# Performance work log

Hardware: AMD Instinct MI355X
Metric: run time of the kernel (lower is better)

The kernel has to match this reference:

```python
import jax, jax.numpy as jnp
import numpy as np

NEG_CAUSAL = -1e10  # matches torch buffer triu(ones*-1e10, diag=1)
NEG_PAD = -10000.0
NUM_HEADS = 16


def setup_inputs() -> dict:
    key = jax.random.key(0)
    ks = jax.random.split(key, 6)
    B, S, D = 2, 2048, 1024
    scale = 0.02
    return {
        "hidden_states": jax.random.normal(ks[0], (B, S, D), jnp.float32),
        "attention_mask": jnp.ones((B, S), jnp.float32),
        "Wq": jax.random.normal(ks[1], (D, D), jnp.float32) * scale,
        "bq": jnp.zeros((D,), jnp.float32),
        "Wk": jax.random.normal(ks[2], (D, D), jnp.float32) * scale,
        "bk": jnp.zeros((D,), jnp.float32),
        "Wv": jax.random.normal(ks[3], (D, D), jnp.float32) * scale,
        "bv": jnp.zeros((D,), jnp.float32),
        "Wo": jax.random.normal(ks[4], (D, D), jnp.float32) * scale,
        "bo": jnp.zeros((D,), jnp.float32),
    }


def reference(hidden_states, attention_mask, Wq, bq, Wk, bk, Wv, bv, Wo, bo):
    B, S, D = hidden_states.shape
    H = NUM_HEADS
    hd = D // H

    def heads(x):  # [B,S,D] -> [B,H,S,hd]
        return x.reshape(B, S, H, hd).transpose(0, 2, 1, 3)

    q = heads(hidden_states @ Wq + bq)
    k = heads(hidden_states @ Wk + bk)
    v = heads(hidden_states @ Wv + bv)

    scores = jnp.einsum("bhqd,bhkd->bhqk", q, k) / jnp.sqrt(jnp.float32(hd))
    causal = jnp.triu(jnp.full((S, S), NEG_CAUSAL, jnp.float32), k=1)
    scores = scores + causal
    # additive padding mask: (1 - m) * -10000, broadcast over heads and query pos
    scores = scores + (1.0 - attention_mask)[:, None, None, :] * NEG_PAD

    probs = jax.nn.softmax(scores, axis=-1)
    # dropout p=0.1 is inactive in eval mode (training=False)
    ctx = jnp.einsum("bhqk,bhkd->bhqd", probs, v)
    ctx = ctx.transpose(0, 2, 1, 3).reshape(B, S, D)
    return ctx @ Wo + bo
```

## Files before the change

kernel.cpp:

```cpp
#include <hip/hip_runtime.h>

typedef __attribute__((ext_vector_type(8))) short short8_t;
typedef __attribute__((ext_vector_type(4))) float float4_t;
typedef unsigned short u16;
typedef unsigned int u32;
typedef unsigned long long u64;

__device__ inline u16 f2bf(float x) {
  union { float f; u32 u; } v; v.f = x;
  u32 r = v.u + 0x7FFFu + ((v.u >> 16) & 1u);
  return (u16)(r >> 16);
}
#if __has_builtin(__builtin_amdgcn_cvt_pk_bf16_f32)
typedef __attribute__((ext_vector_type(2))) __bf16 bf162_t;
__device__ inline u32 pk2(float a, float b) {
  union { bf162_t v; u32 u; } cv;
  cv.v = __builtin_amdgcn_cvt_pk_bf16_f32(a, b);
  return cv.u;
}
#else
__device__ inline u32 pk2(float a, float b) {
  return (u32)f2bf(a) | ((u32)f2bf(b) << 16);
}
#endif

__global__ __launch_bounds__(256) void prologue(const float* __restrict__ X,
                                                const float* __restrict__ Wq, const float* __restrict__ Wk,
                                                const float* __restrict__ Wv, const float* __restrict__ Wo,
                                                u16* __restrict__ Xb, u16* __restrict__ WqkvT,
                                                u16* __restrict__ WoT, const float* __restrict__ maskp,
                                                u32* __restrict__ flags) {
  __shared__ float tls[32][33];
  int bid = blockIdx.x;
  if (bid < 4096) {
    int i = bid * 256 + threadIdx.x;
    float4_t x = ((const float4_t*)X)[i];
    union { u32 u[2]; u64 ll; } o;
    o.u[0] = pk2(x[0], x[1]);
    o.u[1] = pk2(x[2], x[3]);
    ((u64*)Xb)[i] = o.ll;
  } else if (bid < 8192) {
    int t = bid - 4096;
    int mat = t >> 10, tile = t & 1023;
    const float* W = (mat == 0) ? Wq : (mat == 1) ? Wk : (mat == 2) ? Wv : Wo;
    u16* WT = (mat < 3) ? WqkvT + ((size_t)mat << 20) : WoT;
    int tx = threadIdx.x & 31, ty = threadIdx.x >> 5;
    int c0 = (tile & 31) * 32, r0 = (tile >> 5) * 32;
    #pragma unroll
    for (int i = 0; i < 4; ++i)
      tls[ty + i * 8][tx] = W[(r0 + ty + i * 8) * 1024 + c0 + tx];
    __syncthreads();
    #pragma unroll
    for (int i = 0; i < 4; ++i)
      WT[(size_t)(c0 + ty + i * 8) * 1024 + r0 + tx] = f2bf(tls[tx][ty + i * 8]);
  } else {
    int b = bid - 8192;
    const float* mb = maskp + (b << 11) + threadIdx.x * 8;
    bool ok = true;
    #pragma unroll
    for (int i = 0; i < 8; ++i) ok &= (mb[i] == 1.0f);
    u64 bal = __ballot(ok);
    int w = threadIdx.x >> 6;
    if ((threadIdx.x & 63) == 0) tls[0][w] = (bal == ~0ull) ? 1.0f : 0.0f;
    __syncthreads();
    if (threadIdx.x == 0)
      flags[b] = (tls[0][0] != 0.0f && tls[0][1] != 0.0f &&
                  tls[0][2] != 0.0f && tls[0][3] != 0.0f) ? 1u : 0u;
  }
}

__global__ __launch_bounds__(256) void gemm128(const u16* __restrict__ A, const u16* __restrict__ BT,
                                               const float* __restrict__ bias0, const float* __restrict__ bias1,
                                               const float* __restrict__ bias2,
                                               void* __restrict__ o0, void* __restrict__ o1, void* __restrict__ o2,
                                               int mode) {
  __shared__ __align__(16) u16 Als[128 * 64];
  __shared__ __align__(16) u16 Bls[128 * 64];
  int g = blockIdx.x, m0t, n0t;
  if (mode == 4) {
    int mh = g / 384, r = g - mh * 384;
    n0t = r >> 4;
    m0t = mh * 16 + (r & 15);
  } else {
    m0t = g & 31;
    n0t = g >> 5;
  }
  const int m0 = m0t * 128, n0 = n0t * 128;
  const int lane = threadIdx.x & 63, wave = threadIdx.x >> 6;
  const int quad = lane >> 4, c = lane & 15;
  const int wm = wave >> 1, wn = wave & 1;

  const int srow = lane >> 3, schunk = lane & 7;
  int soff[4], dst[4];
  #pragma unroll
  for (int q = 0; q < 4; ++q) {
    int r = wave * 32 + q * 8 + srow;
    soff[q] = r * 1024 + (schunk << 3);
    dst[q]  = r * 64 + ((schunk ^ (r & 7)) << 3);
  }
  const u16* gA = A + (size_t)m0 * 1024;
  const u16* gB = BT + (size_t)n0 * 1024;

  int ar[2][4], br[2][4];
  #pragma unroll
  for (int ko = 0; ko < 2; ++ko) {
    #pragma unroll
    for (int i = 0; i < 4; ++i) {
      int rowa = wm * 64 + i * 16 + c;
      ar[ko][i] = rowa * 64 + (((ko * 4 + quad) ^ (rowa & 7)) << 3);
      int rowb = wn * 64 + i * 16 + c;
      br[ko][i] = rowb * 64 + (((ko * 4 + quad) ^ (rowb & 7)) << 3);
    }
  }

  short8_t ra[4], rb[4];
  #pragma unroll
  for (int q = 0; q < 4; ++q) ra[q] = *(const short8_t*)(gA + soff[q]);
  #pragma unroll
  for (int q = 0; q < 4; ++q) rb[q] = *(const short8_t*)(gB + soff[q]);

  float4_t acc[4][4] = {};
  for (int k0 = 0; k0 < 1024; k0 += 64) {
    #pragma unroll
    for (int q = 0; q < 4; ++q) *(short8_t*)&Als[dst[q]] = ra[q];
    #pragma unroll
    for (int q = 0; q < 4; ++q) *(short8_t*)&Bls[dst[q]] = rb[q];
    __syncthreads();
    if (k0 < 960) {
      #pragma unroll
      for (int q = 0; q < 4; ++q) ra[q] = *(const short8_t*)(gA + soff[q] + k0 + 64);
      #pragma unroll
      for (int q = 0; q < 4; ++q) rb[q] = *(const short8_t*)(gB + soff[q] + k0 + 64);
    }
    #pragma unroll
    for (int ko = 0; ko < 2; ++ko) {
      short8_t af[4], bfr[4];
      #pragma unroll
      for (int i = 0; i < 4; ++i) af[i] = *(const short8_t*)&Als[ar[ko][i]];
      #pragma unroll
      for (int j = 0; j < 4; ++j) bfr[j] = *(const short8_t*)&Bls[br[ko][j]];
      #pragma unroll
      for (int i = 0; i < 4; ++i)
        #pragma unroll
        for (int j = 0; j < 4; ++j)
          acc[i][j] = __builtin_amdgcn_mfma_f32_16x16x32_bf16(af[i], bfr[j], acc[i][j], 0, 0, 0);
    }
    __syncthreads();
  }

  const int mrow = m0 + wm * 64, ncol = n0 + wn * 64;
  if (mode == 3) {
    float* o = (float*)o0;
    #pragma unroll
    for (int i = 0; i < 4; ++i) {
      #pragma unroll
      for (int j = 0; j < 4; ++j) {
        int colb = ncol + j * 16 + c;
        float bv = bias0[colb];
        int rowb = mrow + i * 16 + quad * 4;
        #pragma unroll
        for (int r = 0; r < 4; ++r)
          o[(size_t)(rowb + r) * 1024 + colb] = acc[i][j][r] + bv;
      }
    }
  } else {
    #pragma unroll
    for (int j = 0; j < 4; ++j) {
      int colb = ncol + j * 16 + c;
      int which = colb >> 10;
      int n1 = colb & 1023, h = n1 >> 6, d = n1 & 63;
      const float* bp = (which == 0) ? bias0 : (which == 1 ? bias1 : bias2);
      float bv = bp[n1];
      #pragma unroll
      for (int i = 0; i < 4; ++i) {
        int rowb = mrow + i * 16 + quad * 4;
        int b = rowb >> 11, s = rowb & 2047;
        if (which == 2) {
          u16* o = (u16*)o2 + (((size_t)(b * 16 + h) * 64 + d) * 2048 + s);
          union { u32 u[2]; u64 ll; } ov;
          ov.u[0] = pk2(acc[i][j][0] + bv, acc[i][j][1] + bv);
          ov.u[1] = pk2(acc[i][j][2] + bv, acc[i][j][3] + bv);
          *(u64*)o = ov.ll;
        } else {
          float sc = (which == 0) ? 0.18033688011112042f : 1.0f;
          u16* o = (u16*)((which == 0) ? o0 : o1);
          #pragma unroll
          for (int r = 0; r < 4; ++r)
            o[(((size_t)(b * 16 + h) * 2048 + (s + r)) << 6) + d] = f2bf((acc[i][j][r] + bv) * sc);
        }
      }
    }
  }
}

__device__ inline short8_t p_to_b_swap(const float* p) {
  u32 a0 = pk2(p[0], p[1]), a1 = pk2(p[2], p[3]);
  u32 b0 = pk2(p[4], p[5]), b1 = pk2(p[6], p[7]);
  asm("v_permlane32_swap_b32 %0, %1" : "+v"(a0), "+v"(b0));
  asm("v_permlane32_swap_b32 %0, %1" : "+v"(a1), "+v"(b1));
  asm("v_permlane16_swap_b32 %0, %1" : "+v"(a0), "+v"(b0));
  asm("v_permlane16_swap_b32 %0, %1" : "+v"(a1), "+v"(b1));
  union { u32 u[4]; short8_t v; } pf;
  pf.u[0] = a0; pf.u[1] = a1; pf.u[2] = b0; pf.u[3] = b1;
  return pf.v;
}

__global__ __launch_bounds__(256, 4) void attn_kernel(const u16* __restrict__ Q, const u16* __restrict__ K,
                                                      const u16* __restrict__ VT, const float* __restrict__ mask,
                                                      const u32* __restrict__ flags, u16* __restrict__ ctx) {
  __shared__ __align__(16) u16 Kls[2 * 64 * 64];
  __shared__ __align__(16) u16 Vls[2 * 64 * 64];
  const float C1 = 10000.0f * 1.4426950408889634f;
  int w = threadIdx.x >> 6, lane = threadIdx.x & 63;
  int quad = lane >> 4, c = lane & 15;
  int g = blockIdx.x;
  int bh = (g & 7) * 4 + ((g >> 3) & 3);
  int u = g >> 5;
  int qt = (u < 16) ? (31 - u) : (u - 16);
  int b = bh >> 4, h = bh & 15;
  bool ones = flags && (flags[b] != 0);
  const u16* Kp = K + ((size_t)bh << 17);
  const u16* Vp = VT + ((size_t)bh << 17);
  const float* mp = mask + (b << 11);
  int q0 = qt * 64 + w * 16;

  const u16* Qp = Q + (((size_t)bh * 2048 + q0 + c) << 6) + quad * 8;
  short8_t qf0 = *(const short8_t*)(Qp);
  short8_t qf1 = *(const short8_t*)(Qp + 32);

  const int srow = lane >> 3, schunk = lane & 7;
  const u16* gK[2]; const u16* gV[2]; int dK[2], dV[2];
  #pragma unroll
  for (int i = 0; i < 2; ++i) {
    int R = w * 16 + i * 8 + srow;
    gK[i] = Kp + R * 64 + (schunk << 3);
    dK[i] = R * 64 + ((schunk ^ (R & 7)) << 3);
    gV[i] = Vp + (size_t)R * 2048 + (schunk << 3);
    dV[i] = R * 64 + ((schunk ^ (R & 7)) << 3);
  }

  int koff[4][2];
  #pragma unroll
  for (int kg = 0; kg < 4; ++kg) {
    int r = kg * 16 + c;
    #pragma unroll
    for (int ko = 0; ko < 2; ++ko)
      koff[kg][ko] = r * 64 + (((ko * 4 + quad) ^ (r & 7)) << 3);
  }
  int voff[4][2];
  #pragma unroll
  for (int dblk = 0; dblk < 4; ++dblk) {
    int d = dblk * 16 + c;
    #pragma unroll
    for (int kc = 0; kc < 2; ++kc)
      voff[dblk][kc] = d * 64 + (((kc * 4 + quad) ^ (d & 7)) << 3);
  }

  int ke[8];
  #pragma unroll
  for (int e = 0; e < 8; ++e) ke[e] = ((e >> 2) << 4) + quad * 4 + (e & 3);
  int thr = w * 16 + c;

  float4_t O[4] = {};
  float l = 0.0f;

  short8_t kreg[2], vreg[2];
  #pragma unroll
  for (int i = 0; i < 2; ++i) { kreg[i] = *(const short8_t*)(gK[i]); vreg[i] = *(const short8_t*)(gV[i]); }

  for (int t = 0; t <= qt; ++t) {
    int kb = t << 6;
    int bufo = (t & 1) << 12;
    #pragma unroll
    for (int i = 0; i < 2; ++i) *(short8_t*)&Kls[bufo + dK[i]] = kreg[i];
    #pragma unroll
    for (int i = 0; i < 2; ++i) *(short8_t*)&Vls[bufo + dV[i]] = vreg[i];
    __syncthreads();
    if (t < qt) {
      int kb2 = (t + 1) << 6;
      #pragma unroll
      for (int i = 0; i < 2; ++i) {
        kreg[i] = *(const short8_t*)(gK[i] + (size_t)kb2 * 64);
        vreg[i] = *(const short8_t*)(gV[i] + kb2);
      }
    }
    float4_t s[4];
    #pragma unroll
    for (int kg = 0; kg < 4; ++kg) {
      short8_t k0 = *(const short8_t*)&Kls[bufo + koff[kg][0]];
      short8_t k1 = *(const short8_t*)&Kls[bufo + koff[kg][1]];
      float4_t a = {};
      a = __builtin_amdgcn_mfma_f32_16x16x32_bf16(k0, qf0, a, 0, 0, 0);
      a = __builtin_amdgcn_mfma_f32_16x16x32_bf16(k1, qf1, a, 0, 0, 0);
      s[kg] = a;
    }
    float4_t mpl[4];
    if (!ones) {
      #pragma unroll
      for (int kg = 0; kg < 4; ++kg)
        mpl[kg] = (*(const float4_t*)(mp + kb + kg * 16 + quad * 4) - 1.0f) * C1;
    }
    bool diag = (t == qt);
    short8_t pf[2];
    #pragma unroll
    for (int kc = 0; kc < 2; ++kc) {
      float p[8];
      #pragma unroll
      for (int e = 0; e < 8; ++e) {
        int kg = kc * 2 + (e >> 2);
        p[e] = s[kg][e & 3];
        if (!ones) p[e] += mpl[kg][e & 3];
      }
      if (diag) {
        #pragma unroll
        for (int e = 0; e < 8; ++e) {
          int ko2 = kc * 32 + ke[e];
          p[e] = (ko2 > thr) ? -50.0f : p[e];
        }
      }
      #pragma unroll
      for (int e = 0; e < 8; ++e) {
        float pe = exp2f(p[e]);
        p[e] = pe;
        l += pe;
      }
      pf[kc] = p_to_b_swap(p);
    }
    #pragma unroll
    for (int dblk = 0; dblk < 4; ++dblk) {
      #pragma unroll
      for (int kc = 0; kc < 2; ++kc) {
        short8_t vf = *(const short8_t*)&Vls[bufo + voff[dblk][kc]];
        O[dblk] = __builtin_amdgcn_mfma_f32_16x16x32_bf16(vf, pf[kc], O[dblk], 0, 0, 0);
      }
    }
  }
  l += __shfl_xor(l, 16);
  l += __shfl_xor(l, 32);
  float rl = 1.0f / l;
  u16* op = ctx + ((size_t)(b * 2048 + q0 + c) * 1024 + h * 64 + quad * 4);
  #pragma unroll
  for (int dblk = 0; dblk < 4; ++dblk) {
    union { u32 uu[2]; u64 ll; } ov;
    ov.uu[0] = pk2(O[dblk][0] * rl, O[dblk][1] * rl);
    ov.uu[1] = pk2(O[dblk][2] * rl, O[dblk][3] * rl);
    *(u64*)(op + dblk * 16) = ov.ll;
  }
}

extern "C" void kernel_launch(void* const* d_in, const int* in_sizes, int n_in,
                              void* d_out, int out_size, void* d_ws, size_t ws_size,
                              hipStream_t stream) {
  const float* X    = (const float*)d_in[0];
  const float* mask = (const float*)d_in[1];
  const float* Wq   = (const float*)d_in[2];
  const float* bq   = (const float*)d_in[3];
  const float* Wk   = (const float*)d_in[4];
  const float* bk   = (const float*)d_in[5];
  const float* Wv   = (const float*)d_in[6];
  const float* bv   = (const float*)d_in[7];
  const float* Wo   = (const float*)d_in[8];
  const float* bo   = (const float*)d_in[9];

  char* w = (char*)d_ws;
  u16* Xb     = (u16*)(w);
  u16* WqkvT  = (u16*)(w + (8ull  << 20));
  u16* WoT    = (u16*)(w + (14ull << 20));
  u16* Qb     = (u16*)(w + (16ull << 20));
  u16* Kb     = (u16*)(w + (24ull << 20));
  u16* VTb    = (u16*)(w + (32ull << 20));
  u16* Ctx    = (u16*)(w + (40ull << 20));
  u32* flags  = (ws_size >= (48ull << 20) + 8) ? (u32*)(w + (48ull << 20)) : nullptr;

  prologue<<<flags ? 8194 : 8192, 256, 0, stream>>>(X, Wq, Wk, Wv, Wo, Xb, WqkvT, WoT, mask, flags);
  gemm128<<<768, 256, 0, stream>>>(Xb, WqkvT, bq, bk, bv, Qb, Kb, VTb, 4);
  attn_kernel<<<1024, 256, 0, stream>>>(Qb, Kb, VTb, mask, flags, Ctx);
  gemm128<<<256, 256, 0, stream>>>(Ctx, WoT, bo, bo, bo, d_out, d_out, d_out, 3);
}
```

Measured before the change: 185.7 us.

## Add 64x128-tile output projection GEMM and MFMA priority hints in attention

The output projection now runs in a dedicated kernel with 64x128 tiles, giving 512 blocks instead of 256 so more of the GPU's compute units are busy for the 4096x1024x1024 GEMM. The shared gemm128 loses its mode switch and keeps only the QKV path. In the attention loop, s_setprio raises wave priority around the MFMA sections so matrix work is issued ahead of softmax work on other waves. Smaller tiles mean less data reuse per block and more global loads overall.

Result: no change. 187.4 us (+0.9%).

```diff
diff --git a/kernel.cpp b/kernel.cpp
--- a/kernel.cpp
+++ b/kernel.cpp
@@ -72,19 +72,13 @@
 __global__ __launch_bounds__(256) void gemm128(const u16* __restrict__ A, const u16* __restrict__ BT,
                                                const float* __restrict__ bias0, const float* __restrict__ bias1,
                                                const float* __restrict__ bias2,
-                                               void* __restrict__ o0, void* __restrict__ o1, void* __restrict__ o2,
-                                               int mode) {
+                                               void* __restrict__ o0, void* __restrict__ o1, void* __restrict__ o2) {
   __shared__ __align__(16) u16 Als[128 * 64];
   __shared__ __align__(16) u16 Bls[128 * 64];
-  int g = blockIdx.x, m0t, n0t;
-  if (mode == 4) {
-    int mh = g / 384, r = g - mh * 384;
-    n0t = r >> 4;
-    m0t = mh * 16 + (r & 15);
-  } else {
-    m0t = g & 31;
-    n0t = g >> 5;
-  }
+  int g = blockIdx.x;
+  int mh = g / 384, r = g - mh * 384;
+  int n0t = r >> 4;
+  int m0t = mh * 16 + (r & 15);
   const int m0 = m0t * 128, n0 = n0t * 128;
   const int lane = threadIdx.x & 63, wave = threadIdx.x >> 6;
   const int quad = lane >> 4, c = lane & 15;
@@ -94,9 +88,9 @@
   int soff[4], dst[4];
   #pragma unroll
   for (int q = 0; q < 4; ++q) {
-    int r = wave * 32 + q * 8 + srow;
-    soff[q] = r * 1024 + (schunk << 3);
-    dst[q]  = r * 64 + ((schunk ^ (r & 7)) << 3);
+    int rr = wave * 32 + q * 8 + srow;
+    soff[q] = rr * 1024 + (schunk << 3);
+    dst[q]  = rr * 64 + ((schunk ^ (rr & 7)) << 3);
   }
   const u16* gA = A + (size_t)m0 * 1024;
   const u16* gB = BT + (size_t)n0 * 1024;
@@ -149,46 +143,121 @@
   }
 
   const int mrow = m0 + wm * 64, ncol = n0 + wn * 64;
-  if (mode == 3) {
-    float* o = (float*)o0;
+  #pragma unroll
+  for (int j = 0; j < 4; ++j) {
+    int colb = ncol + j * 16 + c;
+    int which = colb >> 10;
+    int n1 = colb & 1023, h = n1 >> 6, d = n1 & 63;
+    const float* bp = (which == 0) ? bias0 : (which == 1 ? bias1 : bias2);
+    float bv = bp[n1];
     #pragma unroll
     for (int i = 0; i < 4; ++i) {
-      #pragma unroll
-      for (int j = 0; j < 4; ++j) {
-        int colb = ncol + j * 16 + c;
-        float bv = bias0[colb];
-        int rowb = mrow + i * 16 + quad * 4;
+      int rowb = mrow + i * 16 + quad * 4;
+      int b = rowb >> 11, s = rowb & 2047;
+      if (which == 2) {
+        u16* o = (u16*)o2 + (((size_t)(b * 16 + h) * 64 + d) * 2048 + s);
+        union { u32 u[2]; u64 ll; } ov;
+        ov.u[0] = pk2(acc[i][j][0] + bv, acc[i][j][1] + bv);
+        ov.u[1] = pk2(acc[i][j][2] + bv, acc[i][j][3] + bv);
+        *(u64*)o = ov.ll;
+      } else {
+        float sc = (which == 0) ? 0.18033688011112042f : 1.0f;
+        u16* o = (u16*)((which == 0) ? o0 : o1);
         #pragma unroll
-        for (int r = 0; r < 4; ++r)
-          o[(size_t)(rowb + r) * 1024 + colb] = acc[i][j][r] + bv;
-      }
-    }
-  } else {
-    #pragma unroll
-    for (int j = 0; j < 4; ++j) {
-      int colb = ncol + j * 16 + c;
-      int which = colb >> 10;
-      int n1 = colb & 1023, h = n1 >> 6, d = n1 & 63;
-      const float* bp = (which == 0) ? bias0 : (which == 1 ? bias1 : bias2);
-      float bv = bp[n1];
-      #pragma unroll
-      for (int i = 0; i < 4; ++i) {
-        int rowb = mrow + i * 16 + quad * 4;
-        int b = rowb >> 11, s = rowb & 2047;
-        if (which == 2) {
-          u16* o = (u16*)o2 + (((size_t)(b * 16 + h) * 64 + d) * 2048 + s);
-          union { u32 u[2]; u64 ll; } ov;
-          ov.u[0] = pk2(acc[i][j][0] + bv, acc[i][j][1] + bv);
-          ov.u[1] = pk2(acc[i][j][2] + bv, acc[i][j][3] + bv);
-          *(u64*)o = ov.ll;
-        } else {
-          float sc = (which == 0) ? 0.18033688011112042f : 1.0f;
-          u16* o = (u16*)((which == 0) ? o0 : o1);
-          #pragma unroll
-          for (int r = 0; r < 4; ++r)
-            o[(((size_t)(b * 16 + h) * 2048 + (s + r)) << 6) + d] = f2bf((acc[i][j][r] + bv) * sc);
-        }
-      }
+        for (int rr = 0; rr < 4; ++rr)
+          o[(((size_t)(b * 16 + h) * 2048 + (s + rr)) << 6) + d] = f2bf((acc[i][j][rr] + bv) * sc);
+      }
+    }
+  }
+}
+
+__global__ __launch_bounds__(256) void gemm_oproj(const u16* __restrict__ A, const u16* __restrict__ BT,
+                                                  const float* __restrict__ bias, float* __restrict__ o) {
+  __shared__ __align__(16) u16 Als[64 * 64];
+  __shared__ __align__(16) u16 Bls[128 * 64];
+  int g = blockIdx.x;
+  int m0t = g & 63, n0t = g >> 6;
+  const int m0 = m0t * 64, n0 = n0t * 128;
+  const int lane = threadIdx.x & 63, wave = threadIdx.x >> 6;
+  const int quad = lane >> 4, c = lane & 15;
+
+  const int srow = lane >> 3, schunk = lane & 7;
+  int sA[2], dA[2], sB[4], dB[4];
+  #pragma unroll
+  for (int i = 0; i < 2; ++i) {
+    int rr = wave * 16 + i * 8 + srow;
+    sA[i] = rr * 1024 + (schunk << 3);
+    dA[i] = rr * 64 + ((schunk ^ (rr & 7)) << 3);
+  }
+  #pragma unroll
+  for (int q = 0; q < 4; ++q) {
+    int rr = wave * 32 + q * 8 + srow;
+    sB[q] = rr * 1024 + (schunk << 3);
+    dB[q] = rr * 64 + ((schunk ^ (rr & 7)) << 3);
+  }
+  const u16* gA = A + (size_t)m0 * 1024;
+  const u16* gB = BT + (size_t)n0 * 1024;
+
+  int ar[2][4], br[2][2];
+  #pragma unroll
+  for (int ko = 0; ko < 2; ++ko) {
+    #pragma unroll
+    for (int i = 0; i < 4; ++i) {
+      int rowa = i * 16 + c;
+      ar[ko][i] = rowa * 64 + (((ko * 4 + quad) ^ (rowa & 7)) << 3);
+    }
+    #pragma unroll
+    for (int j = 0; j < 2; ++j) {
+      int rowb = wave * 32 + j * 16 + c;
+      br[ko][j] = rowb * 64 + (((ko * 4 + quad) ^ (rowb & 7)) << 3);
+    }
+  }
+
+  short8_t ra[2], rb[4];
+  #pragma unroll
+  for (int i = 0; i < 2; ++i) ra[i] = *(const short8_t*)(gA + sA[i]);
+  #pragma unroll
+  for (int q = 0; q < 4; ++q) rb[q] = *(const short8_t*)(gB + sB[q]);
+
+  float4_t acc[4][2] = {};
+  for (int k0 = 0; k0 < 1024; k0 += 64) {
+    #pragma unroll
+    for (int i = 0; i < 2; ++i) *(short8_t*)&Als[dA[i]] = ra[i];
+    #pragma unroll
+    for (int q = 0; q < 4; ++q) *(short8_t*)&Bls[dB[q]] = rb[q];
+    __syncthreads();
+    if (k0 < 960) {
+      #pragma unroll
+      for (int i = 0; i < 2; ++i) ra[i] = *(const short8_t*)(gA + sA[i] + k0 + 64);
+      #pragma unroll
+      for (int q = 0; q < 4; ++q) rb[q] = *(const short8_t*)(gB + sB[q] + k0 + 64);
+    }
+    #pragma unroll
+    for (int ko = 0; ko < 2; ++ko) {
+      short8_t af[4], bf2[2];
+      #pragma unroll
+      for (int i = 0; i < 4; ++i) af[i] = *(const short8_t*)&Als[ar[ko][i]];
+      #pragma unroll
+      for (int j = 0; j < 2; ++j) bf2[j] = *(const short8_t*)&Bls[br[ko][j]];
+      #pragma unroll
+      for (int i = 0; i < 4; ++i)
+        #pragma unroll
+        for (int j = 0; j < 2; ++j)
+          acc[i][j] = __builtin_amdgcn_mfma_f32_16x16x32_bf16(af[i], bf2[j], acc[i][j], 0, 0, 0);
+    }
+    __syncthreads();
+  }
+
+  #pragma unroll
+  for (int i = 0; i < 4; ++i) {
+    #pragma unroll
+    for (int j = 0; j < 2; ++j) {
+      int colb = n0 + wave * 32 + j * 16 + c;
+      float bv = bias[colb];
+      int rowb = m0 + i * 16 + quad * 4;
+      #pragma unroll
+      for (int rr = 0; rr < 4; ++rr)
+        o[(size_t)(rowb + rr) * 1024 + colb] = acc[i][j][rr] + bv;
     }
   }
 }
@@ -285,6 +354,7 @@
       }
     }
     float4_t s[4];
+    __builtin_amdgcn_s_setprio(1);
     #pragma unroll
     for (int kg = 0; kg < 4; ++kg) {
       short8_t k0 = *(const short8_t*)&Kls[bufo + koff[kg][0]];
@@ -294,6 +364,7 @@
       a = __builtin_amdgcn_mfma_f32_16x16x32_bf16(k1, qf1, a, 0, 0, 0);
       s[kg] = a;
     }
+    __builtin_amdgcn_s_setprio(0);
     float4_t mpl[4];
     if (!ones) {
       #pragma unroll
@@ -326,6 +397,7 @@
       }
       pf[kc] = p_to_b_swap(p);
     }
+    __builtin_amdgcn_s_setprio(1);
     #pragma unroll
     for (int dblk = 0; dblk < 4; ++dblk) {
       #pragma unroll
@@ -334,6 +406,7 @@
         O[dblk] = __builtin_amdgcn_mfma_f32_16x16x32_bf16(vf, pf[kc], O[dblk], 0, 0, 0);
       }
     }
+    __builtin_amdgcn_s_setprio(0);
   }
   l += __shfl_xor(l, 16);
   l += __shfl_xor(l, 32);
@@ -373,7 +446,7 @@
   u32* flags  = (ws_size >= (48ull << 20) + 8) ? (u32*)(w + (48ull << 20)) : nullptr;
 
   prologue<<<flags ? 8194 : 8192, 256, 0, stream>>>(X, Wq, Wk, Wv, Wo, Xb, WqkvT, WoT, mask, flags);
-  gemm128<<<768, 256, 0, stream>>>(Xb, WqkvT, bq, bk, bv, Qb, Kb, VTb, 4);
+  gemm128<<<768, 256, 0, stream>>>(Xb, WqkvT, bq, bk, bv, Qb, Kb, VTb);
   attn_kernel<<<1024, 256, 0, stream>>>(Qb, Kb, VTb, mask, flags, Ctx);
-  gemm128<<<256, 256, 0, stream>>>(Ctx, WoT, bo, bo, bo, d_out, d_out, d_out, 3);
-}
+  gemm_oproj<<<512, 256, 0, stream>>>(Ctx, WoT, bo, (float*)d_out);
+}
```
